# Performance work log

Hardware: AMD Instinct MI355X
Metric: run time of the kernel (lower is better)

Reference implementation:

```python
import jax, jax.numpy as jnp
import numpy as np

D_MOD = 256; H = 8; DH = 32; L_MAX = 96; NUM_MODULES = 15; NUM_TASKS = 7; LN_EPS = 1e-5


def _ln(x, s, b):
    mu = x.mean(-1, keepdims=True)
    v = ((x - mu) ** 2).mean(-1, keepdims=True)
    return (x - mu) * jax.lax.rsqrt(v + LN_EPS) * s + b


def _mha(x, w, b, key_mask, bias):
    # w: [4, D, D] (q,k,v,o), b: [4, D]
    B_, S, _ = x.shape
    q = (x @ w[0] + b[0]).reshape(B_, S, H, DH)
    k = (x @ w[1] + b[1]).reshape(B_, S, H, DH)
    v = (x @ w[2] + b[2]).reshape(B_, S, H, DH)
    logits = jnp.einsum('bihd,bjhd->bhij', q, k) / np.sqrt(DH).astype(np.float32)
    if bias is not None:
        logits = logits + bias
    if key_mask is not None:
        logits = jnp.where(key_mask[:, None, None, :], -1e9, logits)
    a = jax.nn.softmax(logits, axis=-1)
    o = jnp.einsum('bhij,bjhd->bihd', a, v).reshape(B_, S, D_MOD)
    return o @ w[3] + b[3]


def setup_inputs() -> dict:
    key = jax.random.key(0)
    ks = iter(jax.random.split(key, 48))
    B = 64
    M = B * NUM_MODULES  # 960 modules
    lengths = (16 + (np.arange(M) % 81)).astype(np.int32)  # ragged, max 96
    N = int(lengths.sum())  # 53346
    batch_ids = jnp.asarray(np.repeat(np.arange(M), lengths), jnp.int32)
    feats = jax.random.normal(next(ks), (N, D_MOD), jnp.float32)
    coords = jax.random.uniform(next(ks), (N, 3), jnp.float32) * 10.0
    module_to_event = jnp.asarray(np.arange(M) // NUM_MODULES, jnp.int32)
    module_pos = jnp.asarray(np.arange(M) % NUM_MODULES, jnp.int32)
    x_glob = jax.random.normal(next(ks), (B, 16), jnp.float32)

    def nrm(shape):
        return jax.random.normal(next(ks), shape, jnp.float32) * 0.02

    params = dict(
        cls_mod=nrm((1, 1, D_MOD)),
        empty_mod_emb=nrm((D_MOD,)),
        cls_task=nrm((1, NUM_TASKS, D_MOD)),
        pos_emb_table=nrm((1 + NUM_MODULES, D_MOD)),
        mod_attn_w=nrm((2, 4, D_MOD, D_MOD)), mod_attn_b=jnp.zeros((2, 4, D_MOD)),
        mod_rel=nrm((2, H, 3)),
        mod_ln_s=jnp.ones((2, 2, D_MOD)), mod_ln_b=jnp.zeros((2, 2, D_MOD)),
        mod_ffn_w1=nrm((2, D_MOD, 4 * D_MOD)), mod_ffn_b1=jnp.zeros((2, 4 * D_MOD)),
        mod_ffn_w2=nrm((2, 4 * D_MOD, D_MOD)), mod_ffn_b2=jnp.zeros((2, D_MOD)),
        glob_w1=nrm((16, D_MOD)), glob_b1=jnp.zeros((D_MOD,)),
        glob_w2=nrm((D_MOD, D_MOD)), glob_b2=jnp.zeros((D_MOD,)),
        evt_attn_w=nrm((3, 4, D_MOD, D_MOD)), evt_attn_b=jnp.zeros((3, 4, D_MOD)),
        evt_ln_s=jnp.ones((3, 2, D_MOD)), evt_ln_b=jnp.zeros((3, 2, D_MOD)),
        evt_ffn_w1=nrm((3, D_MOD, 2048)), evt_ffn_b1=jnp.zeros((3, 2048)),
        evt_ffn_w2=nrm((3, 2048, D_MOD)), evt_ffn_b2=jnp.zeros((3, D_MOD)),
        head_w=nrm((D_MOD, 16)), head_b=jnp.zeros((16,)),
    )
    return dict(feats=feats, coords=coords, batch_ids=batch_ids,
                module_to_event=module_to_event, module_pos=module_pos,
                x_glob=x_glob, **params)


def reference(feats, coords, batch_ids, module_to_event, module_pos, x_glob,
              cls_mod, empty_mod_emb, cls_task, pos_emb_table,
              mod_attn_w, mod_attn_b, mod_rel, mod_ln_s, mod_ln_b,
              mod_ffn_w1, mod_ffn_b1, mod_ffn_w2, mod_ffn_b2,
              glob_w1, glob_b1, glob_w2, glob_b2,
              evt_attn_w, evt_attn_b, evt_ln_s, evt_ln_b,
              evt_ffn_w1, evt_ffn_b1, evt_ffn_w2, evt_ffn_b2,
              head_w, head_b):
    M = module_to_event.shape[0]
    N = feats.shape[0]
    B = x_glob.shape[0]
    # --- ragged group/pad (pad_sequence over per-module masks) ---
    counts = jax.ops.segment_sum(jnp.ones((N,), jnp.int32), batch_ids, num_segments=M)
    starts = jnp.cumsum(counts) - counts
    pos = jnp.arange(N, dtype=jnp.int32) - starts[batch_ids]  # within-module rank (batch_ids sorted)
    pf = jnp.zeros((M, L_MAX, D_MOD), feats.dtype).at[batch_ids, pos].set(feats)
    pc = jnp.zeros((M, L_MAX, 3), coords.dtype).at[batch_ids, pos].set(coords)
    pad_mask = jnp.arange(L_MAX)[None, :] >= counts[:, None]
    # --- module transformer with relative-position bias, CLS token prepended ---
    seq = jnp.concatenate([jnp.broadcast_to(cls_mod, (M, 1, D_MOD)), pf], axis=1)  # [M,97,256]
    km = jnp.concatenate([jnp.zeros((M, 1), bool), pad_mask], axis=1)
    sc = jnp.concatenate([jnp.zeros((M, 1, 3), coords.dtype), pc], axis=1)
    rel = sc[:, :, None, :] - sc[:, None, :, :]  # [M,S,S,3]
    for l in range(2):
        bias = jnp.einsum('mijc,hc->mhij', rel, mod_rel[l])
        seq = _ln(seq + _mha(seq, mod_attn_w[l], mod_attn_b[l], km, bias), mod_ln_s[l, 0], mod_ln_b[l, 0])
        ff = jax.nn.gelu(seq @ mod_ffn_w1[l] + mod_ffn_b1[l], approximate=False) @ mod_ffn_w2[l] + mod_ffn_b2[l]
        seq = _ln(seq + ff, mod_ln_s[l, 1], mod_ln_b[l, 1])
    mod_emb = seq[:, 0]  # [M,256]
    # --- scatter-assembly into dense per-event tensor ---
    pad_evt = jnp.tile(empty_mod_emb[None, None, :], (B, NUM_MODULES, 1))
    pad_evt = pad_evt.at[module_to_event, module_pos].set(mod_emb)
    glob = (jax.nn.gelu(x_glob @ glob_w1 + glob_b1, approximate=False) @ glob_w2 + glob_b2)[:, None, :]
    se = jnp.concatenate([jnp.broadcast_to(cls_task, (B, NUM_TASKS, D_MOD)), glob, pad_evt], axis=1)  # [B,23,256]
    se = se.at[:, NUM_TASKS:].add(pos_emb_table[None])
    # --- event transformer (post-norm, ReLU FFN d_ff=2048, 3 layers) ---
    for l in range(3):
        se = _ln(se + _mha(se, evt_attn_w[l], evt_attn_b[l], None, None), evt_ln_s[l, 0], evt_ln_b[l, 0])
        ff = jax.nn.relu(se @ evt_ffn_w1[l] + evt_ffn_b1[l]) @ evt_ffn_w2[l] + evt_ffn_b2[l]
        se = _ln(se + ff, evt_ln_s[l, 1], evt_ln_b[l, 1])
    emb = se[:, :NUM_TASKS]

    def head(tok, sl):
        return emb[:, tok] @ head_w[:, sl] + head_b[sl]

    def norml(x):
        return x / jnp.maximum(jnp.linalg.norm(x, axis=-1, keepdims=True), 1e-12)

    sp = jax.nn.softplus
    # order: flavour(4), charm(1), e_vis_cc, e_vis_nc, pt_miss, lep_mag, lep_dir(3), jet_mag, jet_dir(3)
    # NOTE: original code's if/else overwrites flavour/charm with softplus too (replicated).
    out = jnp.concatenate([
        sp(head(0, slice(0, 4))), sp(head(1, slice(4, 5))), sp(head(2, slice(5, 6))),
        sp(head(3, slice(6, 7))), sp(head(4, slice(7, 8))), sp(head(5, slice(8, 9))),
        norml(head(5, slice(9, 12))), sp(head(6, slice(12, 13))), norml(head(6, slice(13, 16)))
    ], axis=-1)  # [B,16]
    return out
```

## Files before the change

### kernel.cpp

```cpp
#include <hip/hip_runtime.h>
#include <hip/hip_bf16.h>
#include <math.h>

typedef unsigned short u16;
typedef unsigned int u32;
typedef __bf16 bf16v8 __attribute__((ext_vector_type(8)));
typedef _Float16 f16v8 __attribute__((ext_vector_type(8)));
typedef __attribute__((ext_vector_type(4))) float f32x4;

#define D_MOD 256
#define NHEAD 8
#define DHEAD 32
#define SEQL 97
#define NTOKE 23

__device__ __forceinline__ float bf2f(u16 u){
  union { unsigned int i; float f; } x; x.i = ((unsigned int)u) << 16; return x.f;
}
__device__ __forceinline__ u16 f2bf(float f){
  return __builtin_bit_cast(u16, (__bf16)f);
}
__device__ __forceinline__ float gelu_fast(float v){
  float z = v * 0.70710678118654752f;
  float az = fabsf(z);
  float t = __builtin_amdgcn_rcpf(fmaf(0.3275911f, az, 1.0f));
  float p = t*(0.254829592f + t*(-0.284496736f + t*(1.421413741f + t*(-1.453152027f + t*1.061405429f))));
  float e = __expf(-z*z);
  float y = 1.0f - p*e;
  float erfz = copysignf(y, z);
  return 0.5f * v * (1.0f + erfz);
}
__device__ __forceinline__ void gld16(const void* g, void* l){
  __builtin_amdgcn_global_load_lds((const __attribute__((address_space(1))) void*)g,
                                   (__attribute__((address_space(3))) void*)l, 16, 0, 0);
}

__global__ __launch_bounds__(256) void prep_t(const float* __restrict__ src, u16* __restrict__ dst,
                                              int K, int N, long sStride, long dStride){
  __shared__ float t[32][33];
  const int k0 = blockIdx.x * 32, n0 = blockIdx.y * 32;
  const float* s = src + (long)blockIdx.z * sStride;
  u16* d = dst + (long)blockIdx.z * dStride;
  const int tx = threadIdx.x & 31, ty = threadIdx.x >> 5;
  #pragma unroll
  for (int r = ty; r < 32; r += 8)
    t[r][tx] = s[(long)(k0 + r) * N + n0 + tx];
  __syncthreads();
  #pragma unroll
  for (int r = ty; r < 32; r += 8)
    d[(long)(n0 + r) * K + k0 + tx] = f2bf(t[tx][r]);
}

__global__ void count_k(const int* __restrict__ bids, int* __restrict__ counts, int n){
  int i = blockIdx.x * blockDim.x + threadIdx.x;
  if (i < n) atomicAdd(&counts[bids[i]], 1);
}

__global__ void scan_k(const int* __restrict__ counts, int* __restrict__ starts, int M){
  __shared__ int buf[1024];
  int t = threadIdx.x;
  int v = (t < M) ? counts[t] : 0;
  buf[t] = v;
  __syncthreads();
  for (int o = 1; o < 1024; o <<= 1){
    int x = (t >= o) ? buf[t - o] : 0;
    __syncthreads();
    buf[t] += x;
    __syncthreads();
  }
  if (t < M) starts[t] = buf[t] - v;
}

__global__ __launch_bounds__(64) void cls_fill(u16* __restrict__ seqc, const float* __restrict__ cls_mod,
                                               const int* __restrict__ starts){
  int m = blockIdx.x, t = threadIdx.x;
  long row = (long)starts[m] + m;
  const float4 v = *(const float4*)(cls_mod + t * 4);
  u16* d = seqc + row * D_MOD + t * 4;
  d[0] = f2bf(v.x); d[1] = f2bf(v.y); d[2] = f2bf(v.z); d[3] = f2bf(v.w);
}

__global__ __launch_bounds__(64) void scatter_k(const float* __restrict__ feats, const float* __restrict__ coords,
                          const int* __restrict__ bids, u16* __restrict__ seqc, float* __restrict__ scc){
  int i = blockIdx.x, t = threadIdx.x;
  long row = (long)i + bids[i] + 1;
  const float4 v = *(const float4*)(feats + (long)i * D_MOD + t * 4);
  u16* d = seqc + row * D_MOD + t * 4;
  d[0] = f2bf(v.x); d[1] = f2bf(v.y); d[2] = f2bf(v.z); d[3] = f2bf(v.w);
  if (t < 3) scc[row * 3 + t] = coords[(long)i * 3 + t];
}

template<int EPI>
__global__ __launch_bounds__(256) void gemm128(
    const u16* __restrict__ A, const u16* __restrict__ Wt,
    const float* __restrict__ bias, const u16* __restrict__ resid,
    u16* __restrict__ C, int K, int N)
{
  __shared__ char smemraw[33792];
  u16* As = (u16*)smemraw;
  u16* Bs = (u16*)(smemraw + 8192);
  float* stg = (float*)smemraw;

  const int tid = threadIdx.x;
  const int w = tid >> 6, l = tid & 63;
  const int wr = w >> 1, wc = w & 1;

  const long nwg = (long)gridDim.x * gridDim.y;
  const long orig = (long)blockIdx.y * gridDim.x + blockIdx.x;
  const long q = nwg >> 3, r = nwg & 7;
  const long xcd = orig & 7, idx = orig >> 3;
  const long swz = (xcd < r ? xcd * (q + 1) : r * (q + 1) + (xcd - r) * q) + idx;
  const int colb = (int)(swz % gridDim.x);
  const long rowb = swz / gridDim.x;
  const long row0 = rowb * 128;
  const int col0 = colb * 128;

  const int fr = l & 15;
  const int ko = (l >> 4) * 8;
  f32x4 acc[4][4] = {};

  const int s0 = w * 128 + l;
  const int s1 = s0 + 64;
  const long ar0 = row0 + (s0 >> 2), ar1 = row0 + (s1 >> 2);
  const long br0 = col0 + (s0 >> 2), br1 = col0 + (s1 >> 2);
  const int cg0 = (s0 & 3) * 8, cg1 = (s1 & 3) * 8;
  u16* ldsA0 = As + w * 1024;
  u16* ldsA1 = As + w * 1024 + 512;
  u16* ldsB0 = Bs + w * 1024;
  u16* ldsB1 = Bs + w * 1024 + 512;

  for (int kt = 0; kt < K; kt += 32){
    __syncthreads();
    gld16(A  + ar0 * K + kt + cg0, ldsA0);
    gld16(A  + ar1 * K + kt + cg1, ldsA1);
    gld16(Wt + br0 * K + kt + cg0, ldsB0);
    gld16(Wt + br1 * K + kt + cg1, ldsB1);
    __syncthreads();
    bf16v8 af[4], bfv[4];
    #pragma unroll
    for (int mi = 0; mi < 4; mi++)
      af[mi] = __builtin_bit_cast(bf16v8, *(const uint4*)(As + (wr*64 + mi*16 + fr)*32 + ko));
    #pragma unroll
    for (int ni = 0; ni < 4; ni++)
      bfv[ni] = __builtin_bit_cast(bf16v8, *(const uint4*)(Bs + (wc*64 + ni*16 + fr)*32 + ko));
    #pragma unroll
    for (int mi = 0; mi < 4; mi++)
      #pragma unroll
      for (int ni = 0; ni < 4; ni++)
        acc[mi][ni] = __builtin_amdgcn_mfma_f32_16x16x32_bf16(af[mi], bfv[ni], acc[mi][ni], 0, 0, 0);
  }

  const int rq = (l >> 4) * 4;
  #pragma unroll
  for (int h = 0; h < 2; h++){
    __syncthreads();
    if (wr == h){
      #pragma unroll
      for (int ni = 0; ni < 4; ni++){
        const int coll = wc*64 + ni*16 + fr;
        const float bb = bias[col0 + coll];
        #pragma unroll
        for (int mi = 0; mi < 4; mi++){
          #pragma unroll
          for (int j = 0; j < 4; j++){
            float v = acc[mi][ni][j] + bb;
            if (EPI == 1) v = gelu_fast(v);
            if (EPI == 2) v = fmaxf(v, 0.0f);
            stg[(mi*16 + rq + j) * 132 + coll] = v;
          }
        }
      }
    }
    __syncthreads();
    #pragma unroll
    for (int i = 0; i < 4; i++){
      const int slot = i * 256 + tid;
      const int rowl = slot >> 4;
      const int cs = (slot & 15) * 8;
      const long gbase = (row0 + h*64 + rowl) * (long)N + col0 + cs;
      float4 lo = *(const float4*)(stg + rowl*132 + cs);
      float4 hi = *(const float4*)(stg + rowl*132 + cs + 4);
      float vv[8] = {lo.x, lo.y, lo.z, lo.w, hi.x, hi.y, hi.z, hi.w};
      if (EPI == 3){
        uint4 rv = *(const uint4*)(resid + gbase);
        const u16* rp = (const u16*)&rv;
        #pragma unroll
        for (int e = 0; e < 8; e++) vv[e] += bf2f(rp[e]);
      }
      uint4 ov;
      u16* op = (u16*)&ov;
      #pragma unroll
      for (int e = 0; e < 8; e++) op[e] = f2bf(vv[e]);
      *(uint4*)(C + gbase) = ov;
    }
  }
}

template<int NT>
__global__ __launch_bounds__(256) void mod_attn_t(
    const u16* __restrict__ qkv, const float* __restrict__ scc,
    const float* __restrict__ rel, const int* __restrict__ counts,
    const int* __restrict__ starts, u16* __restrict__ out, int M, int Slo, int Shi)
{
  constexpr int KS  = (NT + 1) / 2;
  constexpr int NK  = NT * 16;
  constexpr int STR = (KS * 32 <= 64) ? 64 : 128;
  constexpr int PBYTES = (NK * STR * 2 > NK * 132) ? NK * STR * 2 : NK * 132;
  __shared__ char PbRaw[PBYTES];
  __shared__ u16 Vt[32 * STR];
  __shared__ float pj[NK];
  u16* Pb = (u16*)PbRaw;

  const int m = blockIdx.x, h = blockIdx.y;
  const int S = counts[m] + 1;
  if (S <= Slo || S > Shi) return;
  const long base = (long)starts[m] + m;
  const int tid = threadIdx.x, w = tid >> 6, l = tid & 63;
  const int fr = l & 15, ko = (l >> 4) * 8;

  if (tid < NK){
    float v = 1e30f;
    if (tid < S){
      const float* s3 = scc + (base + tid) * 3;
      v = s3[0]*rel[h*3] + s3[1]*rel[h*3+1] + s3[2]*rel[h*3+2];
    }
    pj[tid] = v;
  }
  for (int idx = tid; idx < NK*32; idx += 256){
    int key = idx >> 5, d = idx & 31;
    float v = bf2f(qkv[(base + key)*768 + 512 + h*32 + d]);
    v = fminf(fmaxf(v, -60000.0f), 60000.0f);
    _Float16 hv = (_Float16)v;
    Vt[d*STR + (key ^ ((d & 7) << 3))] = __builtin_bit_cast(u16, hv);
  }
  for (int idx = tid; idx < 32*16; idx += 256){
    int d = idx >> 4, c = NK + (idx & 15);
    Vt[d*STR + (c ^ ((d & 7) << 3))] = 0;
  }
  for (int idx = tid; idx < NK*16; idx += 256){
    int row = idx >> 4, c = NK + (idx & 15);
    Pb[row*STR + (c ^ ((row & 7) << 3))] = 0;
  }
  __syncthreads();

  f32x4 accs[2][NT];
  bf16v8 kf[NT];
  #pragma unroll
  for (int nt = 0; nt < NT; nt++)
    kf[nt] = __builtin_bit_cast(bf16v8, *(const uint4*)(qkv + (base + nt*16 + fr)*768 + 256 + h*32 + ko));
  #pragma unroll
  for (int rr2 = 0; rr2 < 2; rr2++){
    const int rt = w + rr2*4;
    if (rt > NT - 1) break;
    bf16v8 qf = __builtin_bit_cast(bf16v8, *(const uint4*)(qkv + (base + rt*16 + fr)*768 + h*32 + ko));
    #pragma unroll
    for (int nt = 0; nt < NT; nt++){
      f32x4 z = {0.f, 0.f, 0.f, 0.f};
      accs[rr2][nt] = __builtin_amdgcn_mfma_f32_16x16x32_bf16(qf, kf[nt], z, 0, 0, 0);
    }
  }

  float pjr[NT];
  #pragma unroll
  for (int nt = 0; nt < NT; nt++) pjr[nt] = pj[nt*16 + fr];
  const float SCALE = 0.17677669529663687f;
  #pragma unroll
  for (int rr2 = 0; rr2 < 2; rr2++){
    const int rt = w + rr2*4;
    if (rt > NT - 1) break;
    #pragma unroll
    for (int j = 0; j < 4; j++){
      float x[NT], mx = -1e30f;
      #pragma unroll
      for (int nt = 0; nt < NT; nt++){
        x[nt] = accs[rr2][nt][j] * SCALE - pjr[nt];
        mx = fmaxf(mx, x[nt]);
      }
      #pragma unroll
      for (int o = 1; o < 16; o <<= 1) mx = fmaxf(mx, __shfl_xor(mx, o));
      float sum = 0.f;
      #pragma unroll
      for (int nt = 0; nt < NT; nt++){
        x[nt] = __expf(x[nt] - mx);
        sum += x[nt];
      }
      #pragma unroll
      for (int o = 1; o < 16; o <<= 1) sum += __shfl_xor(sum, o);
      const float inv = 1.0f / sum;
      const int row = rt*16 + (l >> 4)*4 + j;
      #pragma unroll
      for (int nt = 0; nt < NT; nt++){
        _Float16 hp = (_Float16)(x[nt] * inv);
        Pb[row*STR + ((nt*16 + fr) ^ ((row & 7) << 3))] = __builtin_bit_cast(u16, hp);
      }
    }
  }
  __syncthreads();

  f32x4 accO[2][2];
  #pragma unroll
  for (int rr2 = 0; rr2 < 2; rr2++){
    const int rt = w + rr2*4;
    if (rt > NT - 1) break;
    #pragma unroll
    for (int nt = 0; nt < 2; nt++){
      f32x4 z = {0.f, 0.f, 0.f, 0.f};
      accO[rr2][nt] = z;
    }
    #pragma unroll
    for (int ks = 0; ks < KS; ks++){
      const int prow = rt*16 + fr;
      f16v8 pa = __builtin_bit_cast(f16v8, *(const uint4*)(Pb + prow*STR + ((ks*32 + ko) ^ ((prow & 7) << 3))));
      #pragma unroll
      for (int nt = 0; nt < 2; nt++){
        const int vrow = nt*16 + fr;
        f16v8 vb = __builtin_bit_cast(f16v8, *(const uint4*)(Vt + vrow*STR + ((ks*32 + ko) ^ ((vrow & 7) << 3))));
        accO[rr2][nt] = __builtin_amdgcn_mfma_f32_16x16x32_f16(pa, vb, accO[rr2][nt], 0, 0, 0);
      }
    }
  }
  __syncthreads();

  float* O = (float*)PbRaw;
  #pragma unroll
  for (int rr2 = 0; rr2 < 2; rr2++){
    const int rt = w + rr2*4;
    if (rt > NT - 1) break;
    #pragma unroll
    for (int nt = 0; nt < 2; nt++)
      #pragma unroll
      for (int j = 0; j < 4; j++)
        O[(rt*16 + (l>>4)*4 + j)*33 + nt*16 + fr] = accO[rr2][nt][j];
  }
  __syncthreads();
  for (int idx = tid; idx < NK*16; idx += 256){
    const int row = idx >> 4;
    if (row >= S) continue;
    const int c = (idx & 15) * 2;
    const float f0 = O[row*33 + c], f1 = O[row*33 + c + 1];
    u32 pk = (u32)f2bf(f0) | ((u32)f2bf(f1) << 16);
    *(u32*)(out + (base + row)*256 + h*32 + c) = pk;
  }
}

__global__ __launch_bounds__(256) void ln_k(u16* __restrict__ x, const float* __restrict__ s,
                                            const float* __restrict__ b, long nrows){
  const long row = (long)blockIdx.x * 4 + (threadIdx.x >> 6);
  if (row >= nrows) return;
  const int t = threadIdx.x & 63;
  u16* xr = x + row * D_MOD;
  uint2 rv = *(const uint2*)(xr + t * 4);
  float v0 = bf2f((u16)(rv.x & 0xffffu));
  float v1 = bf2f((u16)(rv.x >> 16));
  float v2 = bf2f((u16)(rv.y & 0xffffu));
  float v3 = bf2f((u16)(rv.y >> 16));
  float sum = v0 + v1 + v2 + v3;
  float sq  = v0*v0 + v1*v1 + v2*v2 + v3*v3;
  #pragma unroll
  for (int o = 32; o > 0; o >>= 1){
    sum += __shfl_xor(sum, o, 64);
    sq  += __shfl_xor(sq,  o, 64);
  }
  float mu = sum * (1.0f/256.0f);
  float var = sq * (1.0f/256.0f) - mu*mu;
  float rs = rsqrtf(var + 1e-5f);
  int c = t * 4;
  u16 o0 = f2bf((v0-mu)*rs*s[c+0]+b[c+0]);
  u16 o1 = f2bf((v1-mu)*rs*s[c+1]+b[c+1]);
  u16 o2 = f2bf((v2-mu)*rs*s[c+2]+b[c+2]);
  u16 o3 = f2bf((v3-mu)*rs*s[c+3]+b[c+3]);
  uint2 wv;
  wv.x = (unsigned)o0 | ((unsigned)o1 << 16);
  wv.y = (unsigned)o2 | ((unsigned)o3 << 16);
  *(uint2*)(xr + t * 4) = wv;
}

__global__ __launch_bounds__(512, 1) void evt_fused(
    u16* __restrict__ se,
    const u16* __restrict__ attnWT, const float* __restrict__ attnB,
    const u16* __restrict__ f1T, const float* __restrict__ f1B,
    const u16* __restrict__ f2T, const float* __restrict__ f2B,
    const float* __restrict__ lnS, const float* __restrict__ lnB)
{
  __shared__ u16 X[32*264];
  __shared__ u16 Y[32*264];
  __shared__ u16 Sb[8*32*40];
  __shared__ float st1[32*8], st2[32*8];
  __shared__ float muA[32], rsA[32];

  const int b = blockIdx.x;
  const int tid = threadIdx.x, w = tid >> 6, l = tid & 63;
  const int fr = l & 15, hi4 = (l >> 4) * 4, ko = (l >> 4) * 8;
  const long tb = (long)b * NTOKE;
  u16* Sw = Sb + w * 1280;

  for (int idx = tid; idx < 736; idx += 512){
    const int row = idx >> 5, c8 = (idx & 31) * 8;
    *(uint4*)&X[row*264 + c8] = *(const uint4*)(se + (tb + row)*256 + c8);
  }
  for (int idx = tid; idx < 288; idx += 512){
    const int row = 23 + (idx >> 5), c8 = (idx & 31) * 8;
    uint4 z = {0,0,0,0};
    *(uint4*)&X[row*264 + c8] = z;
  }
  __syncthreads();

  for (int lay = 0; lay < 3; lay++){
    const u16*  Wl  = attnWT + (long)lay * 4 * 65536;
    const float* Bl = attnB + lay * 1024;
    const u16*  F1  = f1T + (long)lay * 524288;
    const u16*  F2  = f2T + (long)lay * 524288;

    bf16v8 qf[2], kf[2], pa[2];
    {
      bf16v8 wr_[8][2];
      #pragma unroll
      for (int ks = 0; ks < 8; ks++)
        #pragma unroll
        for (int ct = 0; ct < 2; ct++)
          wr_[ks][ct] = __builtin_bit_cast(bf16v8, *(const uint4*)(Wl + (long)(w*32 + ct*16 + fr)*256 + ks*32 + ko));
      f32x4 acc[2][2] = {};
      #pragma unroll
      for (int ks = 0; ks < 8; ks++){
        bf16v8 a0 = __builtin_bit_cast(bf16v8, *(const uint4*)&X[fr*264 + ks*32 + ko]);
        bf16v8 a1 = __builtin_bit_cast(bf16v8, *(const uint4*)&X[(16+fr)*264 + ks*32 + ko]);
        #pragma unroll
        for (int ct = 0; ct < 2; ct++){
          acc[0][ct] = __builtin_amdgcn_mfma_f32_16x16x32_bf16(a0, wr_[ks][ct], acc[0][ct], 0, 0, 0);
          acc[1][ct] = __builtin_amdgcn_mfma_f32_16x16x32_bf16(a1, wr_[ks][ct], acc[1][ct], 0, 0, 0);
        }
      }
      #pragma unroll
      for (int rt = 0; rt < 2; rt++)
        #pragma unroll
        for (int ct = 0; ct < 2; ct++){
          const float bb = Bl[w*32 + ct*16 + fr];
          #pragma unroll
          for (int j = 0; j < 4; j++)
            Sw[(rt*16 + hi4 + j)*40 + ct*16 + fr] = f2bf(acc[rt][ct][j] + bb);
        }
      qf[0] = __builtin_bit_cast(bf16v8, *(const uint4*)&Sw[fr*40 + ko]);
      qf[1] = __builtin_bit_cast(bf16v8, *(const uint4*)&Sw[(16+fr)*40 + ko]);
    }
    {
      bf16v8 wr_[8][2];
      #pragma unroll
      for (int ks = 0; ks < 8; ks++)
        #pragma unroll
        for (int ct = 0; ct < 2; ct++)
          wr_[ks][ct] = __builtin_bit_cast(bf16v8, *(const uint4*)(Wl + 65536 + (long)(w*32 + ct*16 + fr)*256 + ks*32 + ko));
      f32x4 acc[2][2] = {};
      #pragma unroll
      for (int ks = 0; ks < 8; ks++){
        bf16v8 a0 = __builtin_bit_cast(bf16v8, *(const uint4*)&X[fr*264 + ks*32 + ko]);
        bf16v8 a1 = __builtin_bit_cast(bf16v8, *(const uint4*)&X[(16+fr)*264 + ks*32 + ko]);
        #pragma unroll
        for (int ct = 0; ct < 2; ct++){
          acc[0][ct] = __builtin_amdgcn_mfma_f32_16x16x32_bf16(a0, wr_[ks][ct], acc[0][ct], 0, 0, 0);
          acc[1][ct] = __builtin_amdgcn_mfma_f32_16x16x32_bf16(a1, wr_[ks][ct], acc[1][ct], 0, 0, 0);
        }
      }
      #pragma unroll
      for (int rt = 0; rt < 2; rt++)
        #pragma unroll
        for (int ct = 0; ct < 2; ct++){
          const float bb = Bl[256 + w*32 + ct*16 + fr];
          #pragma unroll
          for (int j = 0; j < 4; j++)
            Sw[(rt*16 + hi4 + j)*40 + ct*16 + fr] = f2bf(acc[rt][ct][j] + bb);
        }
      kf[0] = __builtin_bit_cast(bf16v8, *(const uint4*)&Sw[fr*40 + ko]);
      kf[1] = __builtin_bit_cast(bf16v8, *(const uint4*)&Sw[(16+fr)*40 + ko]);
    }
    {
      f32x4 accS[2][2];
      #pragma unroll
      for (int rt = 0; rt < 2; rt++)
        #pragma unroll
        for (int nt = 0; nt < 2; nt++){
          f32x4 z = {0.f,0.f,0.f,0.f};
          accS[rt][nt] = __builtin_amdgcn_mfma_f32_16x16x32_bf16(qf[rt], kf[nt], z, 0, 0, 0);
        }
      const float SCALE = 0.17677669529663687f;
      const bool v1 = (fr < 7);
      #pragma unroll
      for (int rt = 0; rt < 2; rt++){
        #pragma unroll
        for (int j = 0; j < 4; j++){
          float x0 = accS[rt][0][j] * SCALE;
          float x1 = v1 ? accS[rt][1][j] * SCALE : -1e30f;
          float mx = fmaxf(x0, x1);
          #pragma unroll
          for (int o = 1; o < 16; o <<= 1) mx = fmaxf(mx, __shfl_xor(mx, o));
          float e0 = __expf(x0 - mx);
          float e1 = v1 ? __expf(x1 - mx) : 0.0f;
          float sum = e0 + e1;
          #pragma unroll
          for (int o = 1; o < 16; o <<= 1) sum += __shfl_xor(sum, o);
          const float inv = 1.0f / sum;
          const int row = rt*16 + hi4 + j;
          Sw[row*40 + fr]      = f2bf(e0 * inv);
          Sw[row*40 + 16 + fr] = f2bf(e1 * inv);
        }
      }
      pa[0] = __builtin_bit_cast(bf16v8, *(const uint4*)&Sw[fr*40 + ko]);
      pa[1] = __builtin_bit_cast(bf16v8, *(const uint4*)&Sw[(16+fr)*40 + ko]);
    }
    {
      bf16v8 wr_[8][2];
      #pragma unroll
      for (int ks = 0; ks < 8; ks++)
        #pragma unroll
        for (int ct = 0; ct < 2; ct++)
          wr_[ks][ct] = __builtin_bit_cast(bf16v8, *(const uint4*)(Wl + 131072 + (long)(w*32 + ct*16 + fr)*256 + ks*32 + ko));
      f32x4 acc[2][2] = {};
      #pragma unroll
      for (int ks = 0; ks < 8; ks++){
        bf16v8 a0 = __builtin_bit_cast(bf16v8, *(const uint4*)&X[fr*264 + ks*32 + ko]);
        bf16v8 a1 = __builtin_bit_cast(bf16v8, *(const uint4*)&X[(16+fr)*264 + ks*32 + ko]);
        #pragma unroll
        for (int ct = 0; ct < 2; ct++){
          acc[0][ct] = __builtin_amdgcn_mfma_f32_16x16x32_bf16(a0, wr_[ks][ct], acc[0][ct], 0, 0, 0);
          acc[1][ct] = __builtin_amdgcn_mfma_f32_16x16x32_bf16(a1, wr_[ks][ct], acc[1][ct], 0, 0, 0);
        }
      }
      #pragma unroll
      for (int rt = 0; rt < 2; rt++)
        #pragma unroll
        for (int ct = 0; ct < 2; ct++){
          const float bb = Bl[512 + w*32 + ct*16 + fr];
          u16* dst = &Sw[(ct*16 + fr)*40 + rt*16 + hi4];
          #pragma unroll
          for (int j = 0; j < 4; j++)
            dst[j] = f2bf(acc[rt][ct][j] + bb);
        }
      bf16v8 vb0 = __builtin_bit_cast(bf16v8, *(const uint4*)&Sw[fr*40 + ko]);
      bf16v8 vb1 = __builtin_bit_cast(bf16v8, *(const uint4*)&Sw[(16+fr)*40 + ko]);
      f32x4 accO[2][2];
      #pragma unroll
      for (int rt = 0; rt < 2; rt++){
        f32x4 z = {0.f,0.f,0.f,0.f};
        accO[rt][0] = __builtin_amdgcn_mfma_f32_16x16x32_bf16(pa[rt], vb0, z, 0, 0, 0);
        accO[rt][1] = __builtin_amdgcn_mfma_f32_16x16x32_bf16(pa[rt], vb1, z, 0, 0, 0);
      }
      #pragma unroll
      for (int rt = 0; rt < 2; rt++)
        #pragma unroll
        for (int nt = 0; nt < 2; nt++)
          #pragma unroll
          for (int j = 0; j < 4; j++)
            Y[(rt*16 + hi4 + j)*264 + w*32 + nt*16 + fr] = f2bf(accO[rt][nt][j]);
    }
    __syncthreads();

    {
      bf16v8 wr_[8][2];
      #pragma unroll
      for (int ks = 0; ks < 8; ks++)
        #pragma unroll
        for (int ct = 0; ct < 2; ct++)
          wr_[ks][ct] = __builtin_bit_cast(bf16v8, *(const uint4*)(Wl + 196608 + (long)(w*32 + ct*16 + fr)*256 + ks*32 + ko));
      f32x4 acc[2][2] = {};
      #pragma unroll
      for (int ks = 0; ks < 8; ks++){
        bf16v8 a0 = __builtin_bit_cast(bf16v8, *(const uint4*)&Y[fr*264 + ks*32 + ko]);
        bf16v8 a1 = __builtin_bit_cast(bf16v8, *(const uint4*)&Y[(16+fr)*264 + ks*32 + ko]);
        #pragma unroll
        for (int ct = 0; ct < 2; ct++){
          acc[0][ct] = __builtin_amdgcn_mfma_f32_16x16x32_bf16(a0, wr_[ks][ct], acc[0][ct], 0, 0, 0);
          acc[1][ct] = __builtin_amdgcn_mfma_f32_16x16x32_bf16(a1, wr_[ks][ct], acc[1][ct], 0, 0, 0);
        }
      }
      float val[2][2][4];
      #pragma unroll
      for (int ct = 0; ct < 2; ct++){
        const int col = w*32 + ct*16 + fr;
        const float bb = Bl[768 + col];
        #pragma unroll
        for (int rt = 0; rt < 2; rt++)
          #pragma unroll
          for (int j = 0; j < 4; j++)
            val[rt][ct][j] = acc[rt][ct][j] + bb + bf2f(X[(rt*16 + hi4 + j)*264 + col]);
      }
      #pragma unroll
      for (int rt = 0; rt < 2; rt++)
        #pragma unroll
        for (int j = 0; j < 4; j++){
          float s1 = val[rt][0][j] + val[rt][1][j];
          float s2 = val[rt][0][j]*val[rt][0][j] + val[rt][1][j]*val[rt][1][j];
          #pragma unroll
          for (int o = 1; o < 16; o <<= 1){ s1 += __shfl_xor(s1, o); s2 += __shfl_xor(s2, o); }
          if (fr == 0){
            const int row = rt*16 + hi4 + j;
            st1[row*8 + w] = s1; st2[row*8 + w] = s2;
          }
        }
      __syncthreads();
      if (tid < 32){
        float s1 = 0.f, s2 = 0.f;
        #pragma unroll
        for (int k = 0; k < 8; k++){ s1 += st1[tid*8 + k]; s2 += st2[tid*8 + k]; }
        const float mu = s1 * (1.0f/256.0f);
        const float var = s2 * (1.0f/256.0f) - mu*mu;
        muA[tid] = mu; rsA[tid] = rsqrtf(var + 1e-5f);
      }
      __syncthreads();
      #pragma unroll
      for (int ct = 0; ct < 2; ct++){
        const int col = w*32 + ct*16 + fr;
        const float lw = lnS[lay*512 + col], lb = lnB[lay*512 + col];
        #pragma unroll
        for (int rt = 0; rt < 2; rt++)
          #pragma unroll
          for (int j = 0; j < 4; j++){
            const int row = rt*16 + hi4 + j;
            X[row*264 + col] = f2bf((val[rt][ct][j] - muA[row]) * rsA[row] * lw + lb);
          }
      }
      __syncthreads();
    }

    {
      f32x4 acc2[2][2] = {};
      for (int c = 0; c < 8; c++){
        bf16v8 w1r[8][2];
        #pragma unroll
        for (int ks = 0; ks < 8; ks++)
          #pragma unroll
          for (int ct = 0; ct < 2; ct++)
            w1r[ks][ct] = __builtin_bit_cast(bf16v8, *(const uint4*)(F1 + (long)(c*256 + w*32 + ct*16 + fr)*256 + ks*32 + ko));
        f32x4 acc1[2][2] = {};
        #pragma unroll
        for (int ks = 0; ks < 8; ks++){
          bf16v8 a0 = __builtin_bit_cast(bf16v8, *(const uint4*)&X[fr*264 + ks*32 + ko]);
          bf16v8 a1 = __builtin_bit_cast(bf16v8, *(const uint4*)&X[(16+fr)*264 + ks*32 + ko]);
          #pragma unroll
          for (int ct = 0; ct < 2; ct++){
            acc1[0][ct] = __builtin_amdgcn_mfma_f32_16x16x32_bf16(a0, w1r[ks][ct], acc1[0][ct], 0, 0, 0);
            acc1[1][ct] = __builtin_amdgcn_mfma_f32_16x16x32_bf16(a1, w1r[ks][ct], acc1[1][ct], 0, 0, 0);
          }
        }
        bf16v8 w2r[8][2];
        #pragma unroll
        for (int ks = 0; ks < 8; ks++)
          #pragma unroll
          for (int ct = 0; ct < 2; ct++)
            w2r[ks][ct] = __builtin_bit_cast(bf16v8, *(const uint4*)(F2 + (long)(w*32 + ct*16 + fr)*2048 + c*256 + ks*32 + ko));
        #pragma unroll
        for (int ct = 0; ct < 2; ct++){
          const float bb = f1B[lay*2048 + c*256 + w*32 + ct*16 + fr];
          #pragma unroll
          for (int rt = 0; rt < 2; rt++)
            #pragma unroll
            for (int j = 0; j < 4; j++)
              Y[(rt*16 + hi4 + j)*264 + w*32 + ct*16 + fr] = f2bf(fmaxf(acc1[rt][ct][j] + bb, 0.0f));
        }
        __syncthreads();
        #pragma unroll
        for (int ks = 0; ks < 8; ks++){
          bf16v8 a0 = __builtin_bit_cast(bf16v8, *(const uint4*)&Y[fr*264 + ks*32 + ko]);
          bf16v8 a1 = __builtin_bit_cast(bf16v8, *(const uint4*)&Y[(16+fr)*264 + ks*32 + ko]);
          #pragma unroll
          for (int ct = 0; ct < 2; ct++){
            acc2[0][ct] = __builtin_amdgcn_mfma_f32_16x16x32_bf16(a0, w2r[ks][ct], acc2[0][ct], 0, 0, 0);
            acc2[1][ct] = __builtin_amdgcn_mfma_f32_16x16x32_bf16(a1, w2r[ks][ct], acc2[1][ct], 0, 0, 0);
          }
        }
        __syncthreads();
      }
      float val[2][2][4];
      #pragma unroll
      for (int ct = 0; ct < 2; ct++){
        const int col = w*32 + ct*16 + fr;
        const float bb = f2B[lay*256 + col];
        #pragma unroll
        for (int rt = 0; rt < 2; rt++)
          #pragma unroll
          for (int j = 0; j < 4; j++)
            val[rt][ct][j] = acc2[rt][ct][j] + bb + bf2f(X[(rt*16 + hi4 + j)*264 + col]);
      }
      #pragma unroll
      for (int rt = 0; rt < 2; rt++)
        #pragma unroll
        for (int j = 0; j < 4; j++){
          float s1 = val[rt][0][j] + val[rt][1][j];
          float s2 = val[rt][0][j]*val[rt][0][j] + val[rt][1][j]*val[rt][1][j];
          #pragma unroll
          for (int o = 1; o < 16; o <<= 1){ s1 += __shfl_xor(s1, o); s2 += __shfl_xor(s2, o); }
          if (fr == 0){
            const int row = rt*16 + hi4 + j;
            st1[row*8 + w] = s1; st2[row*8 + w] = s2;
          }
        }
      __syncthreads();
      if (tid < 32){
        float s1 = 0.f, s2 = 0.f;
        #pragma unroll
        for (int k = 0; k < 8; k++){ s1 += st1[tid*8 + k]; s2 += st2[tid*8 + k]; }
        const float mu = s1 * (1.0f/256.0f);
        const float var = s2 * (1.0f/256.0f) - mu*mu;
        muA[tid] = mu; rsA[tid] = rsqrtf(var + 1e-5f);
      }
      __syncthreads();
      #pragma unroll
      for (int ct = 0; ct < 2; ct++){
        const int col = w*32 + ct*16 + fr;
        const float lw = lnS[lay*512 + 256 + col], lb = lnB[lay*512 + 256 + col];
        #pragma unroll
        for (int rt = 0; rt < 2; rt++)
          #pragma unroll
          for (int j = 0; j < 4; j++){
            const int row = rt*16 + hi4 + j;
            X[row*264 + col] = f2bf((val[rt][ct][j] - muA[row]) * rsA[row] * lw + lb);
          }
      }
      __syncthreads();
    }
  }

  for (int idx = tid; idx < 736; idx += 512){
    const int row = idx >> 5, c8 = (idx & 31) * 8;
    *(uint4*)(se + (tb + row)*256 + c8) = *(const uint4*)&X[row*264 + c8];
  }
}

__global__ __launch_bounds__(256) void glob1_k(const float* __restrict__ xg, const float* __restrict__ w1,
                                               const float* __restrict__ b1, u16* __restrict__ h){
  int b = blockIdx.x, d = threadIdx.x;
  float s = b1[d];
  #pragma unroll
  for (int k = 0; k < 16; k++) s += xg[b*16 + k] * w1[k*256 + d];
  h[(long)b*256 + d] = f2bf(gelu_fast(s));
}

__global__ __launch_bounds__(64) void fill_se(u16* __restrict__ se, const float* __restrict__ cls_task,
                                              const u16* __restrict__ globo, const float* __restrict__ pos_emb,
                                              const float* __restrict__ empty_emb){
  int bt = blockIdx.x;
  int b = bt / NTOKE, tk = bt % NTOKE;
  int t = threadIdx.x;
  u16* d = se + (long)bt * D_MOD;
  #pragma unroll
  for (int j = 0; j < 4; j++){
    int c = t*4 + j;
    float v;
    if (tk < 7) v = cls_task[tk*D_MOD + c];
    else if (tk == 7) v = bf2f(globo[(long)b*D_MOD + c]) + pos_emb[c];
    else v = empty_emb[c] + pos_emb[(tk - 7)*D_MOD + c];
    d[c] = f2bf(v);
  }
}

__global__ __launch_bounds__(64) void scatter_mod(u16* __restrict__ se, const u16* __restrict__ seqc,
                                                  const int* __restrict__ m2e, const int* __restrict__ mpos,
                                                  const int* __restrict__ starts,
                                                  const float* __restrict__ pos_emb){
  int m = blockIdx.x, t = threadIdx.x;
  int e = m2e[m], p = mpos[m];
  const u16* src = seqc + ((long)starts[m] + m) * D_MOD;
  u16* dst = se + ((long)e * NTOKE + 8 + p) * D_MOD;
  const float* pe = pos_emb + (long)(1 + p) * D_MOD;
  #pragma unroll
  for (int j = 0; j < 4; j++){
    int c = t*4 + j;
    dst[c] = f2bf(bf2f(src[c]) + pe[c]);
  }
}

__global__ __launch_bounds__(64) void heads_k(const u16* __restrict__ se, const float* __restrict__ hw,
                                              const float* __restrict__ hb, float* __restrict__ out){
  int b = blockIdx.x, t = threadIdx.x;
  __shared__ float raw[16];
  if (t < 16){
    int tok = (t < 4) ? 0 : (t <= 8) ? (t - 3) : (t <= 11) ? 5 : 6;
    const u16* e = se + ((long)b * NTOKE + tok) * D_MOD;
    float s = hb[t];
    for (int d = 0; d < 256; d++) s += bf2f(e[d]) * hw[d*16 + t];
    raw[t] = s;
  }
  __syncthreads();
  if (t < 16){
    float v = raw[t];
    float r;
    if (t <= 8 || t == 12){
      r = fmaxf(v, 0.0f) + log1pf(__expf(-fabsf(v)));
    } else if (t <= 11){
      float n = sqrtf(raw[9]*raw[9] + raw[10]*raw[10] + raw[11]*raw[11]);
      r = v / fmaxf(n, 1e-12f);
    } else {
      float n = sqrtf(raw[13]*raw[13] + raw[14]*raw[14] + raw[15]*raw[15]);
      r = v / fmaxf(n, 1e-12f);
    }
    out[b*16 + t] = r;
  }
}

extern "C" void kernel_launch(void* const* d_in, const int* in_sizes, int n_in,
                              void* d_out, int out_size, void* d_ws, size_t ws_size,
                              hipStream_t stream){
  const float* feats      = (const float*)d_in[0];
  const float* coords     = (const float*)d_in[1];
  const int*   batch_ids  = (const int*)d_in[2];
  const int*   m2e        = (const int*)d_in[3];
  const int*   mpos       = (const int*)d_in[4];
  const float* x_glob     = (const float*)d_in[5];
  const float* cls_mod    = (const float*)d_in[6];
  const float* empty_emb  = (const float*)d_in[7];
  const float* cls_task   = (const float*)d_in[8];
  const float* pos_emb    = (const float*)d_in[9];
  const float* mod_attn_w = (const float*)d_in[10];
  const float* mod_attn_b = (const float*)d_in[11];
  const float* mod_rel    = (const float*)d_in[12];
  const float* mod_ln_s   = (const float*)d_in[13];
  const float* mod_ln_b   = (const float*)d_in[14];
  const float* mod_ffn_w1 = (const float*)d_in[15];
  const float* mod_ffn_b1 = (const float*)d_in[16];
  const float* mod_ffn_w2 = (const float*)d_in[17];
  const float* mod_ffn_b2 = (const float*)d_in[18];
  const float* glob_w1    = (const float*)d_in[19];
  const float* glob_b1    = (const float*)d_in[20];
  const float* glob_w2    = (const float*)d_in[21];
  const float* glob_b2    = (const float*)d_in[22];
  const float* evt_attn_w = (const float*)d_in[23];
  const float* evt_attn_b = (const float*)d_in[24];
  const float* evt_ln_s   = (const float*)d_in[25];
  const float* evt_ln_b   = (const float*)d_in[26];
  const float* evt_ffn_w1 = (const float*)d_in[27];
  const float* evt_ffn_b1 = (const float*)d_in[28];
  const float* evt_ffn_w2 = (const float*)d_in[29];
  const float* evt_ffn_b2 = (const float*)d_in[30];
  const float* head_w     = (const float*)d_in[31];
  const float* head_b     = (const float*)d_in[32];
  float* out = (float*)d_out;

  const int N = in_sizes[0] / 256;
  const int M = in_sizes[3];
  const int B = in_sizes[5] / 16;
  const long CROWS   = (long)M + N;
  const long CROWS_P = (((CROWS + 127) >> 7) << 7) + 128;
  const long TE  = (long)B * NTOKE;

  char* ws = (char*)d_ws;
  u16* modWT   = (u16*)ws;
  u16* evtWT   = modWT + 8L*65536;
  u16* modF1T  = evtWT + 12L*65536;
  u16* modF2T  = modF1T + 2L*262144;
  u16* evtF1T  = modF2T + 2L*262144;
  u16* evtF2T  = evtF1T + 3L*524288;
  u16* globW2T = evtF2T + 3L*524288;
  size_t off = 11468800;
  int* counts = (int*)(ws + off); off += 16*1024;
  int* starts = (int*)(ws + off); off += 16*1024;
  float* scc  = (float*)(ws + off); off += ((size_t)CROWS_P*12 + 255) & ~(size_t)255;
  u16* seqc   = (u16*)(ws + off); off += (size_t)CROWS_P * D_MOD * 2;
  off = (off + 255) & ~(size_t)255;
  const size_t OFF_BIG = off;
  u16* qkv   = (u16*)(ws + OFF_BIG);
  u16* attno = (u16*)(ws + OFF_BIG + (size_t)CROWS_P*768*2);
  u16* ffh   = (u16*)(ws + OFF_BIG);
  u16* se    = (u16*)(ws + OFF_BIG);
  u16* globh = (u16*)(ws + OFF_BIG + 12*1024*1024);
  u16* globo = (u16*)(ws + OFF_BIG + 13*1024*1024);

  prep_t<<<dim3(8, 8, 8),   256, 0, stream>>>(mod_attn_w, modWT,   256, 256,  65536L, 65536L);
  prep_t<<<dim3(8, 8, 12),  256, 0, stream>>>(evt_attn_w, evtWT,   256, 256,  65536L, 65536L);
  prep_t<<<dim3(8, 32, 2),  256, 0, stream>>>(mod_ffn_w1, modF1T,  256, 1024, 262144L, 262144L);
  prep_t<<<dim3(32, 8, 2),  256, 0, stream>>>(mod_ffn_w2, modF2T,  1024, 256, 262144L, 262144L);
  prep_t<<<dim3(8, 64, 3),  256, 0, stream>>>(evt_ffn_w1, evtF1T,  256, 2048, 524288L, 524288L);
  prep_t<<<dim3(64, 8, 3),  256, 0, stream>>>(evt_ffn_w2, evtF2T,  2048, 256, 524288L, 524288L);
  prep_t<<<dim3(8, 8, 1),   256, 0, stream>>>(glob_w2,    globW2T, 256, 256,  65536L, 65536L);

  hipMemsetAsync(counts, 0, (size_t)M*4, stream);
  hipMemsetAsync(scc, 0, (size_t)CROWS_P*12, stream);
  hipMemsetAsync(seqc + CROWS*D_MOD, 0, (size_t)(CROWS_P - CROWS)*D_MOD*2, stream);
  count_k<<<(N + 255)/256, 256, 0, stream>>>(batch_ids, counts, N);
  scan_k<<<1, 1024, 0, stream>>>(counts, starts, M);
  cls_fill<<<M, 64, 0, stream>>>(seqc, cls_mod, starts);
  scatter_k<<<N, 64, 0, stream>>>(feats, coords, batch_ids, seqc, scc);

  const int RB = (int)(CROWS_P / 128);
  for (int l = 0; l < 2; l++){
    gemm128<0><<<dim3(6, RB), 256, 0, stream>>>(seqc, modWT + (long)l*4*65536,
        mod_attn_b + l*1024, nullptr, qkv, 256, 768);
    mod_attn_t<3><<<dim3(M, NHEAD), 256, 0, stream>>>(qkv, scc, mod_rel + l*24, counts, starts, attno, M, 0, 48);
    mod_attn_t<5><<<dim3(M, NHEAD), 256, 0, stream>>>(qkv, scc, mod_rel + l*24, counts, starts, attno, M, 48, 80);
    mod_attn_t<7><<<dim3(M, NHEAD), 256, 0, stream>>>(qkv, scc, mod_rel + l*24, counts, starts, attno, M, 80, 112);
    gemm128<3><<<dim3(2, RB), 256, 0, stream>>>(attno, modWT + ((long)l*4+3)*65536,
        mod_attn_b + l*1024 + 768, seqc, seqc, 256, 256);
    ln_k<<<(int)((CROWS + 3)/4), 256, 0, stream>>>(seqc, mod_ln_s + (l*2)*256, mod_ln_b + (l*2)*256, CROWS);
    gemm128<1><<<dim3(8, RB), 256, 0, stream>>>(seqc, modF1T + (long)l*262144,
        mod_ffn_b1 + l*1024, nullptr, ffh, 256, 1024);
    gemm128<3><<<dim3(2, RB), 256, 0, stream>>>(ffh, modF2T + (long)l*262144,
        mod_ffn_b2 + l*256, seqc, seqc, 1024, 256);
    ln_k<<<(int)((CROWS + 3)/4), 256, 0, stream>>>(seqc, mod_ln_s + (l*2+1)*256, mod_ln_b + (l*2+1)*256, CROWS);
  }

  hipMemsetAsync(globh, 0, 128*256*2, stream);
  glob1_k<<<B, 256, 0, stream>>>(x_glob, glob_w1, glob_b1, globh);
  gemm128<0><<<dim3(2, 1), 256, 0, stream>>>(globh, globW2T, glob_b2, nullptr, globo, 256, 256);
  fill_se<<<(int)TE, 64, 0, stream>>>(se, cls_task, globo, pos_emb, empty_emb);
  scatter_mod<<<M, 64, 0, stream>>>(se, seqc, m2e, mpos, starts, pos_emb);

  evt_fused<<<B, 512, 0, stream>>>(se, evtWT, evt_attn_b, evtF1T, evt_ffn_b1,
                                   evtF2T, evt_ffn_b2, evt_ln_s, evt_ln_b);

  heads_k<<<B, 64, 0, stream>>>(se, head_w, head_b, out);
}
```

Baseline: 991.8 us.

## Software-pipeline event FFN chunks with double-buffered hidden activations

The event-transformer FFN loop is restructured so each iteration computes the second GEMM for chunk c together with the first GEMM for chunk c+1, with a prologue and an epilogue around it. A second shared buffer lets the hidden activations alternate between Y0 and Y1. This cuts the two barriers per chunk down to one and interleaves independent MFMA chains, giving the scheduler more work to hide weight-load and LDS latency. The cost is about 17 KB more shared memory and roughly double the weight registers live at once (w2r plus w1n), which risks spills with 512 threads per block.

New measurement: 1.003 ms. Within noise of the previous version (+1.1%).

```diff
diff --git a/kernel.cpp b/kernel.cpp
--- a/kernel.cpp
+++ b/kernel.cpp
@@ -383,7 +383,8 @@
     const float* __restrict__ lnS, const float* __restrict__ lnB)
 {
   __shared__ u16 X[32*264];
-  __shared__ u16 Y[32*264];
+  __shared__ u16 Y0[32*264];
+  __shared__ u16 Y1[32*264];
   __shared__ u16 Sb[8*32*40];
   __shared__ float st1[32*8], st2[32*8];
   __shared__ float muA[32], rsA[32];
@@ -549,7 +550,7 @@
         for (int nt = 0; nt < 2; nt++)
           #pragma unroll
           for (int j = 0; j < 4; j++)
-            Y[(rt*16 + hi4 + j)*264 + w*32 + nt*16 + fr] = f2bf(accO[rt][nt][j]);
+            Y0[(rt*16 + hi4 + j)*264 + w*32 + nt*16 + fr] = f2bf(accO[rt][nt][j]);
     }
     __syncthreads();
 
@@ -563,8 +564,8 @@
       f32x4 acc[2][2] = {};
       #pragma unroll
       for (int ks = 0; ks < 8; ks++){
-        bf16v8 a0 = __builtin_bit_cast(bf16v8, *(const uint4*)&Y[fr*264 + ks*32 + ko]);
-        bf16v8 a1 = __builtin_bit_cast(bf16v8, *(const uint4*)&Y[(16+fr)*264 + ks*32 + ko]);
+        bf16v8 a0 = __builtin_bit_cast(bf16v8, *(const uint4*)&Y0[fr*264 + ks*32 + ko]);
+        bf16v8 a1 = __builtin_bit_cast(bf16v8, *(const uint4*)&Y0[(16+fr)*264 + ks*32 + ko]);
         #pragma unroll
         for (int ct = 0; ct < 2; ct++){
           acc[0][ct] = __builtin_amdgcn_mfma_f32_16x16x32_bf16(a0, wr_[ks][ct], acc[0][ct], 0, 0, 0);
@@ -622,13 +623,13 @@
 
     {
       f32x4 acc2[2][2] = {};
-      for (int c = 0; c < 8; c++){
+      {
         bf16v8 w1r[8][2];
         #pragma unroll
         for (int ks = 0; ks < 8; ks++)
           #pragma unroll
           for (int ct = 0; ct < 2; ct++)
-            w1r[ks][ct] = __builtin_bit_cast(bf16v8, *(const uint4*)(F1 + (long)(c*256 + w*32 + ct*16 + fr)*256 + ks*32 + ko));
+            w1r[ks][ct] = __builtin_bit_cast(bf16v8, *(const uint4*)(F1 + (long)(w*32 + ct*16 + fr)*256 + ks*32 + ko));
         f32x4 acc1[2][2] = {};
         #pragma unroll
         for (int ks = 0; ks < 8; ks++){
@@ -640,30 +641,73 @@
             acc1[1][ct] = __builtin_amdgcn_mfma_f32_16x16x32_bf16(a1, w1r[ks][ct], acc1[1][ct], 0, 0, 0);
           }
         }
-        bf16v8 w2r[8][2];
-        #pragma unroll
-        for (int ks = 0; ks < 8; ks++)
-          #pragma unroll
-          for (int ct = 0; ct < 2; ct++)
-            w2r[ks][ct] = __builtin_bit_cast(bf16v8, *(const uint4*)(F2 + (long)(w*32 + ct*16 + fr)*2048 + c*256 + ks*32 + ko));
         #pragma unroll
         for (int ct = 0; ct < 2; ct++){
-          const float bb = f1B[lay*2048 + c*256 + w*32 + ct*16 + fr];
+          const float bb = f1B[lay*2048 + w*32 + ct*16 + fr];
           #pragma unroll
           for (int rt = 0; rt < 2; rt++)
             #pragma unroll
             for (int j = 0; j < 4; j++)
-              Y[(rt*16 + hi4 + j)*264 + w*32 + ct*16 + fr] = f2bf(fmaxf(acc1[rt][ct][j] + bb, 0.0f));
+              Y0[(rt*16 + hi4 + j)*264 + w*32 + ct*16 + fr] = f2bf(fmaxf(acc1[rt][ct][j] + bb, 0.0f));
         }
         __syncthreads();
+      }
+      for (int c = 0; c < 7; c++){
+        bf16v8 w2r[8][2];
+        #pragma unroll
+        for (int ks = 0; ks < 8; ks++)
+          #pragma unroll
+          for (int ct = 0; ct < 2; ct++)
+            w2r[ks][ct] = __builtin_bit_cast(bf16v8, *(const uint4*)(F2 + (long)(w*32 + ct*16 + fr)*2048 + c*256 + ks*32 + ko));
+        bf16v8 w1n[8][2];
+        #pragma unroll
+        for (int ks = 0; ks < 8; ks++)
+          #pragma unroll
+          for (int ct = 0; ct < 2; ct++)
+            w1n[ks][ct] = __builtin_bit_cast(bf16v8, *(const uint4*)(F1 + (long)((c+1)*256 + w*32 + ct*16 + fr)*256 + ks*32 + ko));
+        const u16* Ycur = (c & 1) ? Y1 : Y0;
+        u16* Ynxt = (c & 1) ? Y0 : Y1;
+        f32x4 acc1n[2][2] = {};
         #pragma unroll
         for (int ks = 0; ks < 8; ks++){
-          bf16v8 a0 = __builtin_bit_cast(bf16v8, *(const uint4*)&Y[fr*264 + ks*32 + ko]);
-          bf16v8 a1 = __builtin_bit_cast(bf16v8, *(const uint4*)&Y[(16+fr)*264 + ks*32 + ko]);
+          bf16v8 y0 = __builtin_bit_cast(bf16v8, *(const uint4*)&Ycur[fr*264 + ks*32 + ko]);
+          bf16v8 y1 = __builtin_bit_cast(bf16v8, *(const uint4*)&Ycur[(16+fr)*264 + ks*32 + ko]);
+          bf16v8 x0 = __builtin_bit_cast(bf16v8, *(const uint4*)&X[fr*264 + ks*32 + ko]);
+          bf16v8 x1 = __builtin_bit_cast(bf16v8, *(const uint4*)&X[(16+fr)*264 + ks*32 + ko]);
           #pragma unroll
           for (int ct = 0; ct < 2; ct++){
-            acc2[0][ct] = __builtin_amdgcn_mfma_f32_16x16x32_bf16(a0, w2r[ks][ct], acc2[0][ct], 0, 0, 0);
-            acc2[1][ct] = __builtin_amdgcn_mfma_f32_16x16x32_bf16(a1, w2r[ks][ct], acc2[1][ct], 0, 0, 0);
+            acc2[0][ct]  = __builtin_amdgcn_mfma_f32_16x16x32_bf16(y0, w2r[ks][ct], acc2[0][ct], 0, 0, 0);
+            acc2[1][ct]  = __builtin_amdgcn_mfma_f32_16x16x32_bf16(y1, w2r[ks][ct], acc2[1][ct], 0, 0, 0);
+            acc1n[0][ct] = __builtin_amdgcn_mfma_f32_16x16x32_bf16(x0, w1n[ks][ct], acc1n[0][ct], 0, 0, 0);
+            acc1n[1][ct] = __builtin_amdgcn_mfma_f32_16x16x32_bf16(x1, w1n[ks][ct], acc1n[1][ct], 0, 0, 0);
+          }
+        }
+        #pragma unroll
+        for (int ct = 0; ct < 2; ct++){
+          const float bb = f1B[lay*2048 + (c+1)*256 + w*32 + ct*16 + fr];
+          #pragma unroll
+          for (int rt = 0; rt < 2; rt++)
+            #pragma unroll
+            for (int j = 0; j < 4; j++)
+              Ynxt[(rt*16 + hi4 + j)*264 + w*32 + ct*16 + fr] = f2bf(fmaxf(acc1n[rt][ct][j] + bb, 0.0f));
+        }
+        __syncthreads();
+      }
+      {
+        bf16v8 w2r[8][2];
+        #pragma unroll
+        for (int ks = 0; ks < 8; ks++)
+          #pragma unroll
+          for (int ct = 0; ct < 2; ct++)
+            w2r[ks][ct] = __builtin_bit_cast(bf16v8, *(const uint4*)(F2 + (long)(w*32 + ct*16 + fr)*2048 + 7*256 + ks*32 + ko));
+        #pragma unroll
+        for (int ks = 0; ks < 8; ks++){
+          bf16v8 y0 = __builtin_bit_cast(bf16v8, *(const uint4*)&Y1[fr*264 + ks*32 + ko]);
+          bf16v8 y1 = __builtin_bit_cast(bf16v8, *(const uint4*)&Y1[(16+fr)*264 + ks*32 + ko]);
+          #pragma unroll
+          for (int ct = 0; ct < 2; ct++){
+            acc2[0][ct] = __builtin_amdgcn_mfma_f32_16x16x32_bf16(y0, w2r[ks][ct], acc2[0][ct], 0, 0, 0);
+            acc2[1][ct] = __builtin_amdgcn_mfma_f32_16x16x32_bf16(y1, w2r[ks][ct], acc2[1][ct], 0, 0, 0);
           }
         }
         __syncthreads();
```
